# Optimization experiments

Hardware: AMD Instinct MI355X
Metric: run time of the kernel (lower is better)

The kernel has to match this reference:

```python
import jax, jax.numpy as jnp
import numpy as np

RANK, A1, A2, B1, B2 = 64, 64, 64, 64, 64
N_TOKENS = 8192


def _xavier_uniform(key, shape, fan_in, fan_out, dtype=jnp.float32):
    bound = float(np.sqrt(6.0 / (fan_in + fan_out)))
    return jax.random.uniform(key, shape, dtype, -bound, bound)


def setup_inputs() -> dict:
    key = jax.random.key(0)
    kx, ka, kb, kbias = jax.random.split(key, 4)
    x = jax.random.normal(kx, (N_TOKENS, A1 * B1), dtype=jnp.float32)
    # torch xavier on a 3D tensor (rank, d1, d2): fan_in = d1*d2, fan_out = rank*d2
    a = _xavier_uniform(ka, (RANK, A1, A2), A1 * A2, RANK * A2)
    b = _xavier_uniform(kb, (RANK, B1, B2), B1 * B2, RANK * B2)
    bias = jax.random.normal(kbias, (A2 * B2,), dtype=jnp.float32)
    return {"x": x, "a": a, "b": b, "bias": bias}


def reference(x, a, b, bias):
    r, a1, a2 = a.shape
    _, b1, b2 = b.shape
    # w = sum_r kron(a_r, b_r):  w[i*b1+k, j*b2+l] = sum_r a[r,i,j] * b[r,k,l]
    w = jnp.einsum('rij,rkl->ikjl', a, b).reshape(a1 * b1, a2 * b2)
    out = x @ w  # (N, a2*b2)
    return out + bias[None, :]
```

## Files before the change

kernel.cpp:

```cpp
#include <hip/hip_runtime.h>
#include <hip/hip_bf16.h>


#define M_DIM 8192
#define N_DIM 4096
#define K_DIM 4096
#define KT_COUNT 128

typedef __attribute__((ext_vector_type(8))) short short8;
typedef __attribute__((ext_vector_type(4))) float floatx4;

typedef __attribute__((address_space(1))) void gvoid_t;
typedef __attribute__((address_space(3))) void lvoid_t;

static __device__ __forceinline__ void gl_lds16(const void* g, const void* l) {
  __builtin_amdgcn_global_load_lds((gvoid_t*)(unsigned long long)g,
                                   (lvoid_t*)(unsigned int)(unsigned long long)l,
                                   16, 0, 0);
}

static __device__ __forceinline__ unsigned short f2bf(float f) {
  unsigned int u = __builtin_bit_cast(unsigned int, f);
  u = (u + 0x7fffu + ((u >> 16) & 1u)) >> 16;
  return (unsigned short)u;
}

__global__ __launch_bounds__(256) void prep_kernel(
    const float* __restrict__ x, const float* __restrict__ a,
    const float* __restrict__ b, unsigned short* __restrict__ Xp,
    unsigned short* __restrict__ Wp) {
  __shared__ float lds[128 * 33];
  const int bid = blockIdx.x;
  const int t = threadIdx.x;

  if (bid < 2048) {
    const int rg = bid & 255;
    const int i = rg >> 2;
    const int j0 = (rg & 3) * 16;
    const int k0 = (bid >> 8) * 8;

    {
      const int r = t >> 2, jq = t & 3;
      float4 v = ((const float4*)(a + (size_t)r * 4096 + i * 64 + j0))[jq];
      ((float4*)lds)[r * 4 + jq] = v;
    }
    __syncthreads();

    const int l = t & 63;
    const int jj = t >> 6;
    float acc[4][8];
#pragma unroll
    for (int jp = 0; jp < 4; ++jp)
#pragma unroll
      for (int kb = 0; kb < 8; ++kb) acc[jp][kb] = 0.f;

    const float* bb = b + k0 * 64 + l;
#pragma unroll 4
    for (int r = 0; r < 64; ++r) {
      float4 aj = ((const float4*)lds)[r * 4 + jj];
      float bv[8];
#pragma unroll
      for (int kb = 0; kb < 8; ++kb) bv[kb] = bb[(size_t)r * 4096 + kb * 64];
      const float av[4] = {aj.x, aj.y, aj.z, aj.w};
#pragma unroll
      for (int jp = 0; jp < 4; ++jp)
#pragma unroll
        for (int kb = 0; kb < 8; ++kb)
          acc[jp][kb] = fmaf(av[jp], bv[kb], acc[jp][kb]);
    }

    const int kt = (i * 64 + k0) >> 5;
    const int c = (k0 & 31) >> 3;
#pragma unroll
    for (int jp = 0; jp < 4; ++jp) {
      const int j = j0 + jj * 4 + jp;
      const int n = j * 64 + l;
      const int blob = (n >> 7) * KT_COUNT + kt;
      const int pos = c * 128 + (n & 127);
      short8 o;
#pragma unroll
      for (int kb = 0; kb < 8; ++kb) o[kb] = (short)f2bf(acc[jp][kb]);
      *(short8*)(Wp + (size_t)blob * 4096 + pos * 8) = o;
    }
  } else {
    const int pid = bid - 2048;
    const int kt = pid & 127;
    const int M0 = pid >> 7;

    {
      const int row = t >> 1;
      const int half = t & 1;
      const float* src = x + (size_t)(M0 * 128 + row) * K_DIM + kt * 32 + half * 16;
      float v[16];
#pragma unroll
      for (int w = 0; w < 4; ++w) {
        float4 vv = ((const float4*)src)[w];
        v[w * 4 + 0] = vv.x; v[w * 4 + 1] = vv.y;
        v[w * 4 + 2] = vv.z; v[w * 4 + 3] = vv.w;
      }
#pragma unroll
      for (int e = 0; e < 16; ++e) lds[row * 33 + half * 16 + e] = v[e];
    }
    __syncthreads();

    unsigned short* dst = Xp + (size_t)(M0 * KT_COUNT + kt) * 4096;
#pragma unroll
    for (int q = 0; q < 2; ++q) {
      const int p = q * 256 + t;
      const int c = p >> 7, mm = p & 127;
      short8 o;
#pragma unroll
      for (int j = 0; j < 8; ++j) o[j] = (short)f2bf(lds[mm * 33 + c * 8 + j]);
      *(short8*)(dst + p * 8) = o;
    }
  }
}

__global__ __launch_bounds__(256) void gemm_kernel(
    const unsigned short* __restrict__ Xp, const unsigned short* __restrict__ Wp,
    const float* __restrict__ bias, float* __restrict__ out) {
  __shared__ short8 As[512];
  __shared__ short8 Bs[512];

  const int bid = blockIdx.x;
  const int xcd = bid & 7;
  const int pos = bid >> 3;
  const int N0 = xcd * 4 + (pos & 3);
  const int M0 = pos >> 2;

  const int t = threadIdx.x;
  const int wave = t >> 6, lane = t & 63;
  const int l16 = lane & 15, quad = lane >> 4;
  const int wm = wave & 1, wn = wave >> 1;

  floatx4 acc[4][4];
#pragma unroll
  for (int mt = 0; mt < 4; ++mt)
#pragma unroll
    for (int nt = 0; nt < 4; ++nt) acc[mt][nt] = (floatx4){0.f, 0.f, 0.f, 0.f};

  const unsigned short* pa = Xp + (size_t)M0 * KT_COUNT * 4096 + (size_t)t * 8;
  const unsigned short* pb = Wp + (size_t)N0 * KT_COUNT * 4096 + (size_t)t * 8;
  const short8* lA0 = As + wave * 64;
  const short8* lA1 = As + 256 + wave * 64;
  const short8* lB0 = Bs + wave * 64;
  const short8* lB1 = Bs + 256 + wave * 64;

  for (int kt = 0; kt < KT_COUNT; ++kt) {
    __syncthreads();
    gl_lds16(pa, lA0);
    gl_lds16(pa + 2048, lA1);
    gl_lds16(pb, lB0);
    gl_lds16(pb + 2048, lB1);
    pa += 4096;
    pb += 4096;
    __syncthreads();

    short8 af[4], bf[4];
#pragma unroll
    for (int mt = 0; mt < 4; ++mt)
      af[mt] = As[quad * 128 + wm * 64 + mt * 16 + l16];
#pragma unroll
    for (int nt = 0; nt < 4; ++nt)
      bf[nt] = Bs[quad * 128 + wn * 64 + nt * 16 + l16];
#pragma unroll
    for (int mt = 0; mt < 4; ++mt)
#pragma unroll
      for (int nt = 0; nt < 4; ++nt)
        acc[mt][nt] = __builtin_amdgcn_mfma_f32_16x16x32_bf16(
            af[mt], bf[nt], acc[mt][nt], 0, 0, 0);
  }

  const int col_base = N0 * 128 + wn * 64;
  const int row_base = M0 * 128 + wm * 64;
#pragma unroll
  for (int nt = 0; nt < 4; ++nt) {
    const int col = col_base + nt * 16 + l16;
    const float bv = bias[col];
#pragma unroll
    for (int mt = 0; mt < 4; ++mt) {
      floatx4 v = acc[mt][nt];
#pragma unroll
      for (int r4 = 0; r4 < 4; ++r4) {
        const int row = row_base + mt * 16 + quad * 4 + r4;
        out[(size_t)row * N_DIM + col] = v[r4] + bv;
      }
    }
  }
}

extern "C" void kernel_launch(void* const* d_in, const int* in_sizes, int n_in,
                              void* d_out, int out_size, void* d_ws, size_t ws_size,
                              hipStream_t stream) {
  const float* x = (const float*)d_in[0];
  const float* a = (const float*)d_in[1];
  const float* b = (const float*)d_in[2];
  const float* bias = (const float*)d_in[3];
  float* out = (float*)d_out;

  unsigned short* Xp = (unsigned short*)d_ws;
  unsigned short* Wp = Xp + (size_t)M_DIM * K_DIM;

  prep_kernel<<<2048 + 8192, 256, 0, stream>>>(x, a, b, Xp, Wp);
  gemm_kernel<<<2048, 256, 0, stream>>>(Xp, Wp, bias, out);
}
```

Before: 512.0 us.

## Enlarge GEMM tile to 256x256 with 8 waves and 4-stage LDS prefetch pipeline

```diff
diff --git a/kernel.cpp b/kernel.cpp
--- a/kernel.cpp
+++ b/kernel.cpp
@@ -116,69 +116,111 @@
   }
 }
 
-__global__ __launch_bounds__(256) void gemm_kernel(
+#define BAR() asm volatile("s_barrier" ::: "memory")
+#define WAIT_VM(N) asm volatile("s_waitcnt vmcnt(" #N ")" ::: "memory")
+#define WAIT_LGKM0() asm volatile("s_waitcnt lgkmcnt(0)" ::: "memory")
+
+__global__ __launch_bounds__(512, 2) void gemm_kernel(
     const unsigned short* __restrict__ Xp, const unsigned short* __restrict__ Wp,
     const float* __restrict__ bias, float* __restrict__ out) {
-  __shared__ short8 As[512];
-  __shared__ short8 Bs[512];
+  __shared__ short8 As[4][2][512];
+  __shared__ short8 Bs[4][2][512];
 
   const int bid = blockIdx.x;
   const int xcd = bid & 7;
   const int pos = bid >> 3;
-  const int N0 = xcd * 4 + (pos & 3);
-  const int M0 = pos >> 2;
+  const int N0 = xcd * 2 + (pos & 1);
+  const int M0 = pos >> 1;
 
   const int t = threadIdx.x;
   const int wave = t >> 6, lane = t & 63;
   const int l16 = lane & 15, quad = lane >> 4;
-  const int wm = wave & 1, wn = wave >> 1;
-
-  floatx4 acc[4][4];
-#pragma unroll
-  for (int mt = 0; mt < 4; ++mt)
+  const int wm = wave & 1;
+  const int wn = wave >> 1;
+
+  floatx4 acc[8][4];
+#pragma unroll
+  for (int mt = 0; mt < 8; ++mt)
 #pragma unroll
     for (int nt = 0; nt < 4; ++nt) acc[mt][nt] = (floatx4){0.f, 0.f, 0.f, 0.f};
 
-  const unsigned short* pa = Xp + (size_t)M0 * KT_COUNT * 4096 + (size_t)t * 8;
-  const unsigned short* pb = Wp + (size_t)N0 * KT_COUNT * 4096 + (size_t)t * 8;
-  const short8* lA0 = As + wave * 64;
-  const short8* lA1 = As + 256 + wave * 64;
-  const short8* lB0 = Bs + wave * 64;
-  const short8* lB1 = Bs + 256 + wave * 64;
-
+  const unsigned short* gA0 = Xp + (size_t)(M0 * 2 + 0) * KT_COUNT * 4096 + (size_t)t * 8;
+  const unsigned short* gA1 = Xp + (size_t)(M0 * 2 + 1) * KT_COUNT * 4096 + (size_t)t * 8;
+  const unsigned short* gB0 = Wp + (size_t)(N0 * 2 + 0) * KT_COUNT * 4096 + (size_t)t * 8;
+  const unsigned short* gB1 = Wp + (size_t)(N0 * 2 + 1) * KT_COUNT * 4096 + (size_t)t * 8;
+
+  gl_lds16(gA0, &As[0][0][t]);
+  gl_lds16(gA1, &As[0][1][t]);
+  gl_lds16(gB0, &Bs[0][0][t]);
+  gl_lds16(gB1, &Bs[0][1][t]);
+  gl_lds16(gA0 + 4096, &As[1][0][t]);
+  gl_lds16(gA1 + 4096, &As[1][1][t]);
+  gl_lds16(gB0 + 4096, &Bs[1][0][t]);
+  gl_lds16(gB1 + 4096, &Bs[1][1][t]);
+  WAIT_VM(4);
+  BAR();
+
+  const int ra = quad * 128 + l16;
+  const int rb = quad * 128 + (wn & 1) * 64 + l16;
+  const int bh = wn >> 1;
+
+#pragma unroll 2
   for (int kt = 0; kt < KT_COUNT; ++kt) {
-    __syncthreads();
-    gl_lds16(pa, lA0);
-    gl_lds16(pa + 2048, lA1);
-    gl_lds16(pb, lB0);
-    gl_lds16(pb + 2048, lB1);
-    pa += 4096;
-    pb += 4096;
-    __syncthreads();
-
-    short8 af[4], bf[4];
-#pragma unroll
-    for (int mt = 0; mt < 4; ++mt)
-      af[mt] = As[quad * 128 + wm * 64 + mt * 16 + l16];
-#pragma unroll
-    for (int nt = 0; nt < 4; ++nt)
-      bf[nt] = Bs[quad * 128 + wn * 64 + nt * 16 + l16];
-#pragma unroll
-    for (int mt = 0; mt < 4; ++mt)
+    const int tb = kt & 3;
+    const int db = (kt + 2) & 3;
+    const size_t soff =
+        (size_t)((kt + 2 < KT_COUNT) ? kt + 2 : KT_COUNT - 1) * 4096;
+
+    short8 bf[4], af[4];
+
+#pragma unroll
+    for (int nt = 0; nt < 4; ++nt) bf[nt] = Bs[tb][bh][rb + nt * 16];
+#pragma unroll
+    for (int m = 0; m < 4; ++m) af[m] = As[tb][wm][ra + m * 16];
+    gl_lds16(gA0 + soff, &As[db][0][t]);
+    gl_lds16(gA1 + soff, &As[db][1][t]);
+    BAR();
+    WAIT_LGKM0();
+    __builtin_amdgcn_sched_barrier(0);
+    __builtin_amdgcn_s_setprio(1);
+#pragma unroll
+    for (int m = 0; m < 4; ++m)
 #pragma unroll
       for (int nt = 0; nt < 4; ++nt)
-        acc[mt][nt] = __builtin_amdgcn_mfma_f32_16x16x32_bf16(
-            af[mt], bf[nt], acc[mt][nt], 0, 0, 0);
+        acc[m][nt] = __builtin_amdgcn_mfma_f32_16x16x32_bf16(
+            af[m], bf[nt], acc[m][nt], 0, 0, 0);
+    __builtin_amdgcn_s_setprio(0);
+    __builtin_amdgcn_sched_barrier(0);
+    BAR();
+
+#pragma unroll
+    for (int m = 0; m < 4; ++m) af[m] = As[tb][wm][ra + (4 + m) * 16];
+    gl_lds16(gB0 + soff, &Bs[db][0][t]);
+    gl_lds16(gB1 + soff, &Bs[db][1][t]);
+    WAIT_VM(4);
+    BAR();
+    WAIT_LGKM0();
+    __builtin_amdgcn_sched_barrier(0);
+    __builtin_amdgcn_s_setprio(1);
+#pragma unroll
+    for (int m = 0; m < 4; ++m)
+#pragma unroll
+      for (int nt = 0; nt < 4; ++nt)
+        acc[4 + m][nt] = __builtin_amdgcn_mfma_f32_16x16x32_bf16(
+            af[m], bf[nt], acc[4 + m][nt], 0, 0, 0);
+    __builtin_amdgcn_s_setprio(0);
+    __builtin_amdgcn_sched_barrier(0);
+    BAR();
   }
 
-  const int col_base = N0 * 128 + wn * 64;
-  const int row_base = M0 * 128 + wm * 64;
+  const int col_base = N0 * 256 + wn * 64;
+  const int row_base = M0 * 256 + wm * 128;
 #pragma unroll
   for (int nt = 0; nt < 4; ++nt) {
     const int col = col_base + nt * 16 + l16;
     const float bv = bias[col];
 #pragma unroll
-    for (int mt = 0; mt < 4; ++mt) {
+    for (int mt = 0; mt < 8; ++mt) {
       floatx4 v = acc[mt][nt];
 #pragma unroll
       for (int r4 = 0; r4 < 4; ++r4) {
@@ -202,5 +244,5 @@
   unsigned short* Wp = Xp + (size_t)M_DIM * K_DIM;
 
   prep_kernel<<<2048 + 8192, 256, 0, stream>>>(x, a, b, Xp, Wp);
-  gemm_kernel<<<2048, 256, 0, stream>>>(Xp, Wp, bias, out);
-}
+  gemm_kernel<<<512, 512, 0, stream>>>(Xp, Wp, bias, out);
+}
```

After: 480.5 us. -6.1%, faster.
